# Performance work log

Hardware: AMD Instinct MI355X
Metric: run time of the kernel (lower is better)

The kernel has to match this reference:

```python
import jax, jax.numpy as jnp
import numpy as np

SOFTMAX_T = 0.01
TOPK_CLIP = 3
SCORE_THR = 0.01
IOU_THR = 0.5
CLIP_RATIO = 0.65
OBJ_RATIO = 0.35
PRE_TOP = 1000   # pre-NMS candidates kept from the N*C (proposal, class) grid
MAX_OUT = 300    # max detections per image (padded)


def setup_inputs() -> dict:
    key = jax.random.key(0)
    k1, k2, k3, k4, k5 = jax.random.split(key, 5)
    B, N, D, C = 8, 1000, 512, 1203
    pe = jax.random.normal(k1, (B, N, D), jnp.float32)
    obj = jax.random.uniform(k2, (B, N), jnp.float32)
    xy = jax.random.uniform(k3, (B, N, 2), jnp.float32) * 900.0
    wh = jax.random.uniform(k4, (B, N, 2), jnp.float32) * 100.0 + 1.0
    boxes = jnp.concatenate([xy, xy + wh], axis=-1)  # valid x1y1x2y2
    ce = jax.random.normal(k5, (C, D), jnp.float32)
    image_ids = jnp.arange(B, dtype=jnp.int32)
    return {"proposal_embeddings": pe, "proposal_objectness": obj,
            "proposal_bboxes": boxes, "class_embeddings": ce,
            "image_ids": image_ids}


def _pairwise_iou(b):
    # b: [K, 4] in x1y1x2y2
    x1, y1, x2, y2 = b[:, 0], b[:, 1], b[:, 2], b[:, 3]
    area = jnp.maximum(x2 - x1, 0.0) * jnp.maximum(y2 - y1, 0.0)
    iw = jnp.maximum(jnp.minimum(x2[:, None], x2[None, :]) - jnp.maximum(x1[:, None], x1[None, :]), 0.0)
    ih = jnp.maximum(jnp.minimum(y2[:, None], y2[None, :]) - jnp.maximum(y1[:, None], y1[None, :]), 0.0)
    inter = iw * ih
    union = area[:, None] + area[None, :] - inter
    return inter / jnp.maximum(union, 1e-6)


def _nms_single(boxes, scores):
    # boxes: [N, 4], scores: [N, C] -> fixed-shape multiclass NMS
    N, C = scores.shape
    flat = scores.reshape(-1)                      # [N*C]
    s = jnp.where(flat > SCORE_THR, flat, -1.0)
    top_s, top_i = jax.lax.top_k(s, PRE_TOP)       # sorted desc
    lab = top_i % C
    pid = top_i // C
    b = boxes[pid]                                 # [K, 4]
    valid = top_s > SCORE_THR
    iou = _pairwise_iou(b)                         # [K, K]
    sup_mat = (iou > IOU_THR) & (lab[:, None] == lab[None, :])
    idx = jnp.arange(PRE_TOP)

    def body(i, keep):
        sup = sup_mat[i] & keep[i] & (idx > i)     # a kept box suppresses lower-scored same-class overlaps
        return keep & ~sup

    keep = jax.lax.fori_loop(0, PRE_TOP, body, valid)
    kept = jnp.where(keep, top_s, -1.0)
    fs, fi = jax.lax.top_k(kept, MAX_OUT)
    fvalid = fs > SCORE_THR
    fb = jnp.where(fvalid[:, None], b[fi], 0.0)
    bbox5 = jnp.concatenate([fb, jnp.where(fvalid, fs, 0.0)[:, None]], axis=-1)
    flab = jnp.where(fvalid, lab[fi], -1)
    return bbox5, flab, fvalid


def reference(proposal_embeddings, proposal_objectness, proposal_bboxes, class_embeddings, image_ids):
    pe = proposal_embeddings / jnp.linalg.norm(proposal_embeddings, axis=2, keepdims=True)
    logit = jax.nn.softmax(jnp.einsum('bnd,cd->bnc', pe, class_embeddings) / SOFTMAX_T, axis=2)
    v = jax.lax.top_k(logit, TOPK_CLIP)[0]         # [B, N, TOPK]
    clip_k = logit * (logit >= v[..., -1:])
    final = clip_k * CLIP_RATIO + (clip_k > 0) * proposal_objectness[..., None] * OBJ_RATIO
    bbox5, labels, valid = jax.vmap(_nms_single)(proposal_bboxes, final)
    img = jnp.where(valid, image_ids[:, None], -1)
    B = bbox5.shape[0]
    return bbox5.reshape(B * MAX_OUT, 5), labels.reshape(-1), img.reshape(-1)
```

## Files before the change

kernel.cpp:

```cpp
#include <hip/hip_runtime.h>
#include <stdint.h>

typedef unsigned long long u64;
typedef unsigned int u32;

#define BIMG 8
#define NPROP 1000
#define DDIM 512
#define CCLS 1203
#define MAXOUT 300
#define CSLOT 4096
#define TRIW 8665
#define CTI 1204

__device__ __forceinline__ u32 flipf(float f) {
  u32 u = __float_as_uint(f);
  return (u & 0x80000000u) ? ~u : (u | 0x80000000u);
}
__device__ __forceinline__ float unflipf(u32 x) {
  u32 u = (x & 0x80000000u) ? (x ^ 0x80000000u) : ~x;
  return __uint_as_float(u);
}
__device__ __forceinline__ void push3(float v, float& a0, float& a1, float& a2) {
  if (v > a0) { a2 = a1; a1 = a0; a0 = v; }
  else if (v > a1) { a2 = a1; a1 = v; }
  else if (v > a2) { a2 = v; }
}

__global__ __launch_bounds__(128) void transpose_cei(
    const float* __restrict__ ce, float4* __restrict__ ceTi)
{
  const int c = blockIdx.x;
  const int t = threadIdx.x;
  float4 v = *((const float4*)(ce + (size_t)c * DDIM) + t);
  ceTi[(size_t)t * CTI + c] = v;
}

__global__ __launch_bounds__(512) void score_kernel_i(
    const float* __restrict__ pe, const float* __restrict__ obj,
    const float4* __restrict__ ceTi, u64* __restrict__ cand)
{
  __shared__ float pe_s[8][DDIM];
  __shared__ float red2[8];
  __shared__ float trip2[8][3];
  __shared__ u64 rowc[8][16];
  __shared__ u32 rcnt[8];

  const int tid = threadIdx.x;
  const int lane = tid & 63, wv = tid >> 6;
  const int blk = blockIdx.x;
  const int b = blk / 125;
  const int n0 = (blk % 125) * 8;

  {
    const float4* src = (const float4*)(pe + (size_t)(b * NPROP + n0) * DDIM);
    float4* dst = (float4*)&pe_s[0][0];
    for (int i = tid; i < 1024; i += 512) dst[i] = src[i];
  }
  if (tid < 8) rcnt[tid] = 0u;
  __syncthreads();

  float nrm[8];
  #pragma unroll 1
  for (int r = 0; r < 8; r++) {
    float s = 0.f;
    if (tid < 256) {
      float x0 = pe_s[r][tid], x1 = pe_s[r][tid + 256];
      s = x0 * x0 + x1 * x1;
    }
    #pragma unroll
    for (int off = 32; off; off >>= 1) s += __shfl_xor(s, off);
    if (lane == 0 && wv < 4) red2[wv] = s;
    __syncthreads();
    nrm[r] = sqrtf(((red2[0] + red2[1]) + red2[2]) + red2[3]);
    __syncthreads();
  }
  if (tid < 256) {
    #pragma unroll
    for (int r = 0; r < 8; r++) {
      pe_s[r][tid]       = __fdiv_rn(pe_s[r][tid], nrm[r]);
      pe_s[r][tid + 256] = __fdiv_rn(pe_s[r][tid + 256], nrm[r]);
    }
  }
  __syncthreads();

  const bool has3 = (tid < 179);
  const int c2c = has3 ? (1024 + tid) : 1202;

  float acc[3][8];
  #pragma unroll
  for (int k = 0; k < 3; k++)
    #pragma unroll
    for (int r = 0; r < 8; r++) acc[k][r] = 0.f;

  const float4* ps4 = (const float4*)&pe_s[0][0];
  const float4* pA = ceTi + tid;
  const float4* pB = ceTi + 512 + tid;
  const float4* pC = ceTi + c2c;
  for (int d4 = 0; d4 < 128; d4++) {
    float4 bA = pA[(size_t)d4 * CTI];
    float4 bB = pB[(size_t)d4 * CTI];
    float4 bC = pC[(size_t)d4 * CTI];
    #pragma unroll
    for (int r = 0; r < 8; r++) {
      float4 a = ps4[r * 128 + d4];
      acc[0][r] = fmaf(a.x, bA.x, acc[0][r]); acc[0][r] = fmaf(a.y, bA.y, acc[0][r]);
      acc[0][r] = fmaf(a.z, bA.z, acc[0][r]); acc[0][r] = fmaf(a.w, bA.w, acc[0][r]);
      acc[1][r] = fmaf(a.x, bB.x, acc[1][r]); acc[1][r] = fmaf(a.y, bB.y, acc[1][r]);
      acc[1][r] = fmaf(a.z, bB.z, acc[1][r]); acc[1][r] = fmaf(a.w, bB.w, acc[1][r]);
      acc[2][r] = fmaf(a.x, bC.x, acc[2][r]); acc[2][r] = fmaf(a.y, bC.y, acc[2][r]);
      acc[2][r] = fmaf(a.z, bC.z, acc[2][r]); acc[2][r] = fmaf(a.w, bC.w, acc[2][r]);
    }
  }

  #pragma unroll
  for (int k = 0; k < 3; k++)
    #pragma unroll
    for (int r = 0; r < 8; r++) acc[k][r] = __fdiv_rn(acc[k][r], 0.01f);

  #pragma unroll 1
  for (int r = 0; r < 8; r++) {
    const float l0 = acc[0][r], l1 = acc[1][r];
    const float l2 = has3 ? acc[2][r] : -INFINITY;

    float t0 = -INFINITY, t1 = -INFINITY, t2 = -INFINITY;
    push3(l0, t0, t1, t2); push3(l1, t0, t1, t2); push3(l2, t0, t1, t2);
    #pragma unroll
    for (int off = 32; off; off >>= 1) {
      float u0 = __shfl_xor(t0, off);
      float u1 = __shfl_xor(t1, off);
      float u2 = __shfl_xor(t2, off);
      push3(u0, t0, t1, t2); push3(u1, t0, t1, t2); push3(u2, t0, t1, t2);
    }
    if (lane == 0) { trip2[wv][0] = t0; trip2[wv][1] = t1; trip2[wv][2] = t2; }
    __syncthreads();
    float a0 = -INFINITY, a1 = -INFINITY, a2 = -INFINITY;
    #pragma unroll
    for (int w = 0; w < 8; w++) {
      push3(trip2[w][0], a0, a1, a2);
      push3(trip2[w][1], a0, a1, a2);
      push3(trip2[w][2], a0, a1, a2);
    }
    const float m = a0, s3 = a2;

    float ls = expf(l0 - m);
    ls += expf(l1 - m);
    ls += expf(l2 - m);
    #pragma unroll
    for (int off = 32; off; off >>= 1) ls += __shfl_xor(ls, off);
    if (lane == 0) red2[wv] = ls;
    __syncthreads();
    float sm = red2[0];
    #pragma unroll
    for (int w = 1; w < 8; w++) sm += red2[w];

    const float v3 = __fdiv_rn(expf(s3 - m), sm);
    const float objv = obj[b * NPROP + n0 + r];

    #pragma unroll
    for (int k = 0; k < 3; k++) {
      if (k == 2 && !has3) continue;
      const float lk = (k == 0) ? l0 : (k == 1) ? l1 : l2;
      const float p = __fdiv_rn(expf(lk - m), sm);
      if (p >= v3 && p > 0.f) {
        const float sc = __fadd_rn(__fmul_rn(p, 0.65f), __fmul_rn(objv, 0.35f));
        if (sc > 0.01f) {
          const int c = (k == 0) ? tid : (k == 1) ? (512 + tid) : (1024 + tid);
          u32 flat = (u32)(n0 + r) * (u32)CCLS + (u32)c;
          u64 key = (((u64)flipf(sc)) << 32) | (u32)(~flat);
          u32 slot = atomicAdd(&rcnt[r], 1u);
          if (slot < 16u) rowc[r][slot] = key;
        }
      }
    }
    __syncthreads();
  }

  if (tid < 8) {
    int n = (int)rcnt[tid]; if (n > 16) n = 16;
    for (int a3 = 1; a3 < n; a3++) {
      u64 kx = rowc[tid][a3]; int bp = a3 - 1;
      while (bp >= 0 && rowc[tid][bp] < kx) { rowc[tid][bp + 1] = rowc[tid][bp]; bp--; }
      rowc[tid][bp + 1] = kx;
    }
    int mth = n < 4 ? n : 4;
    u64* dst = cand + (size_t)b * CSLOT + (size_t)(n0 + tid) * 4;
    for (int s2 = 0; s2 < mth; s2++) dst[s2] = rowc[tid][s2];
  }
}

__global__ __launch_bounds__(256, 2) void score_kernel(
    const float* __restrict__ pe, const float* __restrict__ obj,
    const float* __restrict__ ce, u64* __restrict__ cand)
{
  __shared__ float pe_s[8][DDIM];
  __shared__ float red[4][8];
  __shared__ float trip[4][8][3];
  __shared__ u64 rowc[8][16];
  __shared__ u32 rcnt[8];

  const int tid = threadIdx.x;
  const int lane = tid & 63, wv = tid >> 6;
  const int blk = blockIdx.x;
  const int b = blk / 125;
  const int n0 = (blk % 125) * 8;

  {
    const float4* src = (const float4*)(pe + (size_t)(b * NPROP + n0) * DDIM);
    float4* dst = (float4*)&pe_s[0][0];
    for (int i = tid; i < 1024; i += 256) dst[i] = src[i];
  }
  if (tid < 8) rcnt[tid] = 0u;
  __syncthreads();

  float nrm[8];
  #pragma unroll
  for (int r = 0; r < 8; r++) {
    float x0 = pe_s[r][tid], x1 = pe_s[r][tid + 256];
    float s = x0 * x0 + x1 * x1;
    #pragma unroll
    for (int off = 32; off; off >>= 1) s += __shfl_xor(s, off);
    if (lane == 0) red[wv][r] = s;
  }
  __syncthreads();
  #pragma unroll
  for (int r = 0; r < 8; r++)
    nrm[r] = sqrtf(((red[0][r] + red[1][r]) + red[2][r]) + red[3][r]);
  __syncthreads();
  #pragma unroll
  for (int r = 0; r < 8; r++) {
    pe_s[r][tid]       = __fdiv_rn(pe_s[r][tid], nrm[r]);
    pe_s[r][tid + 256] = __fdiv_rn(pe_s[r][tid + 256], nrm[r]);
  }
  __syncthreads();

  const int c4 = 1024 + tid;
  const bool v4 = (c4 < CCLS);
  const float4* ceb = (const float4*)ce;
  const float4* pc0 = ceb + (size_t)(tid)       * 128;
  const float4* pc1 = ceb + (size_t)(tid + 256) * 128;
  const float4* pc2 = ceb + (size_t)(tid + 512) * 128;
  const float4* pc3 = ceb + (size_t)(tid + 768) * 128;
  const float4* pc4 = ceb + (size_t)(v4 ? c4 : (CCLS - 1)) * 128;

  float acc[5][8];
  #pragma unroll
  for (int k = 0; k < 5; k++)
    #pragma unroll
    for (int r = 0; r < 8; r++) acc[k][r] = 0.f;

  const float4* ps4 = (const float4*)&pe_s[0][0];
  for (int d4 = 0; d4 < 128; d4++) {
    float4 bv0 = pc0[d4], bv1 = pc1[d4], bv2 = pc2[d4], bv3 = pc3[d4], bv4 = pc4[d4];
    #pragma unroll
    for (int r = 0; r < 8; r++) {
      float4 a = ps4[r * 128 + d4];
      acc[0][r] = fmaf(a.x, bv0.x, acc[0][r]); acc[0][r] = fmaf(a.y, bv0.y, acc[0][r]);
      acc[0][r] = fmaf(a.z, bv0.z, acc[0][r]); acc[0][r] = fmaf(a.w, bv0.w, acc[0][r]);
      acc[1][r] = fmaf(a.x, bv1.x, acc[1][r]); acc[1][r] = fmaf(a.y, bv1.y, acc[1][r]);
      acc[1][r] = fmaf(a.z, bv1.z, acc[1][r]); acc[1][r] = fmaf(a.w, bv1.w, acc[1][r]);
      acc[2][r] = fmaf(a.x, bv2.x, acc[2][r]); acc[2][r] = fmaf(a.y, bv2.y, acc[2][r]);
      acc[2][r] = fmaf(a.z, bv2.z, acc[2][r]); acc[2][r] = fmaf(a.w, bv2.w, acc[2][r]);
      acc[3][r] = fmaf(a.x, bv3.x, acc[3][r]); acc[3][r] = fmaf(a.y, bv3.y, acc[3][r]);
      acc[3][r] = fmaf(a.z, bv3.z, acc[3][r]); acc[3][r] = fmaf(a.w, bv3.w, acc[3][r]);
      acc[4][r] = fmaf(a.x, bv4.x, acc[4][r]); acc[4][r] = fmaf(a.y, bv4.y, acc[4][r]);
      acc[4][r] = fmaf(a.z, bv4.z, acc[4][r]); acc[4][r] = fmaf(a.w, bv4.w, acc[4][r]);
    }
  }

  #pragma unroll
  for (int k = 0; k < 5; k++)
    #pragma unroll
    for (int r = 0; r < 8; r++) acc[k][r] = __fdiv_rn(acc[k][r], 0.01f);
  if (!v4) {
    #pragma unroll
    for (int r = 0; r < 8; r++) acc[4][r] = -INFINITY;
  }

  float t0[8], t1[8], t2[8];
  #pragma unroll
  for (int r = 0; r < 8; r++) {
    t0[r] = t1[r] = t2[r] = -INFINITY;
    push3(acc[0][r], t0[r], t1[r], t2[r]);
    push3(acc[1][r], t0[r], t1[r], t2[r]);
    push3(acc[2][r], t0[r], t1[r], t2[r]);
    push3(acc[3][r], t0[r], t1[r], t2[r]);
    push3(acc[4][r], t0[r], t1[r], t2[r]);
  }
  #pragma unroll
  for (int off = 32; off; off >>= 1) {
    #pragma unroll
    for (int r = 0; r < 8; r++) {
      float u0 = __shfl_xor(t0[r], off);
      float u1 = __shfl_xor(t1[r], off);
      float u2 = __shfl_xor(t2[r], off);
      push3(u0, t0[r], t1[r], t2[r]);
      push3(u1, t0[r], t1[r], t2[r]);
      push3(u2, t0[r], t1[r], t2[r]);
    }
  }
  if (lane == 0) {
    #pragma unroll
    for (int r = 0; r < 8; r++) {
      trip[wv][r][0] = t0[r]; trip[wv][r][1] = t1[r]; trip[wv][r][2] = t2[r];
    }
  }
  __syncthreads();
  float m[8], s3[8];
  #pragma unroll
  for (int r = 0; r < 8; r++) {
    float a0 = -INFINITY, a1 = -INFINITY, a2 = -INFINITY;
    #pragma unroll
    for (int w = 0; w < 4; w++) {
      push3(trip[w][r][0], a0, a1, a2);
      push3(trip[w][r][1], a0, a1, a2);
      push3(trip[w][r][2], a0, a1, a2);
    }
    m[r] = a0; s3[r] = a2;
  }

  float sm[8];
  #pragma unroll
  for (int r = 0; r < 8; r++) {
    float ls = expf(acc[0][r] - m[r]);
    ls += expf(acc[1][r] - m[r]);
    ls += expf(acc[2][r] - m[r]);
    ls += expf(acc[3][r] - m[r]);
    ls += expf(acc[4][r] - m[r]);
    #pragma unroll
    for (int off = 32; off; off >>= 1) ls += __shfl_xor(ls, off);
    if (lane == 0) red[wv][r] = ls;
  }
  __syncthreads();
  #pragma unroll
  for (int r = 0; r < 8; r++)
    sm[r] = ((red[0][r] + red[1][r]) + red[2][r]) + red[3][r];

  float v3[8], objv[8];
  #pragma unroll
  for (int r = 0; r < 8; r++) {
    v3[r] = __fdiv_rn(expf(s3[r] - m[r]), sm[r]);
    objv[r] = obj[b * NPROP + n0 + r];
  }

  #pragma unroll
  for (int k = 0; k < 5; k++) {
    if (k == 4 && !v4) continue;
    const int c = tid + (k << 8);
    #pragma unroll
    for (int r = 0; r < 8; r++) {
      float e = expf(acc[k][r] - m[r]);
      float p = __fdiv_rn(e, sm[r]);
      if (p >= v3[r] && p > 0.f) {
        float sc = __fadd_rn(__fmul_rn(p, 0.65f), __fmul_rn(objv[r], 0.35f));
        if (sc > 0.01f) {
          u32 flat = (u32)(n0 + r) * (u32)CCLS + (u32)c;
          u64 key = (((u64)flipf(sc)) << 32) | (u32)(~flat);
          u32 slot = atomicAdd(&rcnt[r], 1u);
          if (slot < 16u) rowc[r][slot] = key;
        }
      }
    }
  }
  __syncthreads();
  if (tid < 8) {
    int n = (int)rcnt[tid]; if (n > 16) n = 16;
    for (int a2 = 1; a2 < n; a2++) {
      u64 kx = rowc[tid][a2]; int bp = a2 - 1;
      while (bp >= 0 && rowc[tid][bp] < kx) { rowc[tid][bp + 1] = rowc[tid][bp]; bp--; }
      rowc[tid][bp + 1] = kx;
    }
    int mth = n < 4 ? n : 4;
    u64* dst = cand + (size_t)b * CSLOT + (size_t)(n0 + tid) * 4;
    for (int s2 = 0; s2 < mth; s2++) dst[s2] = rowc[tid][s2];
  }
}

__global__ __launch_bounds__(1024) void sort_kernel(u64* __restrict__ cand)
{
  __shared__ u64 s[CSLOT];
  const int tid = threadIdx.x;
  u64* cb = cand + (size_t)blockIdx.x * CSLOT;
  for (int i = tid; i < CSLOT; i += 1024) s[i] = cb[i];
  __syncthreads();
  for (int k = 2; k <= CSLOT; k <<= 1) {
    for (int j = k >> 1; j > 0; j >>= 1) {
      for (int i = tid; i < CSLOT; i += 1024) {
        int ixj = i ^ j;
        if (ixj > i) {
          u64 a = s[i], c = s[ixj];
          if (((i & k) == 0) ? (a < c) : (a > c)) { s[i] = c; s[ixj] = a; }
        }
      }
      __syncthreads();
    }
  }
  for (int i = tid; i < CSLOT; i += 1024) cb[i] = s[i];
}

__global__ __launch_bounds__(1024) void nms_fused(
    const u64* __restrict__ cand, const float* __restrict__ boxes,
    const int* __restrict__ image_ids, float* __restrict__ out)
{
  __shared__ u64 supw[TRIW];
  __shared__ float4 bx[NPROP];
  __shared__ float ar[NPROP];
  __shared__ float scs[NPROP];
  __shared__ int lbs[NPROP];

  const int tid = threadIdx.x;
  const int b = blockIdx.x;

  for (int i = tid; i < NPROP; i += 1024) {
    u64 key = cand[(size_t)b * CSLOT + i];
    float sc = -1.0f; int pid = 0, lab = -1;
    if (key != 0ull) {
      sc = unflipf((u32)(key >> 32));
      u32 flat = ~(u32)key;
      pid = (int)(flat / (u32)CCLS);
      lab = (int)(flat % (u32)CCLS);
    }
    float4 v = ((const float4*)boxes)[b * NPROP + pid];
    bx[i] = v;
    ar[i] = __fmul_rn(fmaxf(__fsub_rn(v.z, v.x), 0.f),
                      fmaxf(__fsub_rn(v.w, v.y), 0.f));
    scs[i] = sc;
    lbs[i] = lab;
  }
  __syncthreads();

  for (int i = tid; i < NPROP; i += 1024) {
    float4 bi = bx[i]; float ai = ar[i]; int li = lbs[i];
    int g = i >> 6, t = i - (g << 6);
    int rb = 16 * i - (32 * g * (g - 1) + g * (t + 1));
    int w0 = (i + 1) >> 6;
    for (int w = w0; w < 16; w++) {
      u64 bits = 0;
      int jb = w << 6;
      int ts = (w == g) ? (t + 1) : 0;
      int te = NPROP - jb; if (te > 64) te = 64;
      for (int tt = ts; tt < te; tt++) {
        int j = jb + tt;
        if (lbs[j] != li) continue;
        float4 bj = bx[j];
        float iw = fmaxf(__fsub_rn(fminf(bi.z, bj.z), fmaxf(bi.x, bj.x)), 0.f);
        float ih = fmaxf(__fsub_rn(fminf(bi.w, bj.w), fmaxf(bi.y, bj.y)), 0.f);
        float inter = __fmul_rn(iw, ih);
        if (inter <= 0.f) continue;
        float uni = __fsub_rn(__fadd_rn(ai, ar[j]), inter);
        if (__fdiv_rn(inter, fmaxf(uni, 1e-6f)) > 0.5f) bits |= (1ull << tt);
      }
      supw[rb + w - w0] = bits;
    }
  }
  __syncthreads();

  for (int j = tid; j < MAXOUT * 5; j += 1024)
    out[(size_t)b * MAXOUT * 5 + j] = 0.f;
  for (int j = tid; j < MAXOUT; j += 1024) {
    out[BIMG * MAXOUT * 5 + b * MAXOUT + j] = -1.f;
    out[BIMG * MAXOUT * 6 + b * MAXOUT + j] = -1.f;
  }
  __syncthreads();

  if (tid >= 64) return;
  const int lane = tid, myw = lane & 15;

  u64 keep = 0;
  if (lane < 16) {
    #pragma unroll 4
    for (int t = 0; t < 64; t++) {
      int i = (lane << 6) + t;
      if (i < NPROP && scs[i] > 0.01f) keep |= (1ull << t);
    }
  }

  auto LDROW = [&](int i) -> u64 {
    if (i >= NPROP || lane >= 16) return 0ull;
    int g = i >> 6, t = i & 63;
    int w0 = (i + 1) >> 6;
    if (myw < w0) return 0ull;
    int rb = 16 * i - (32 * g * (g - 1) + g * (t + 1));
    return supw[rb + myw - w0];
  };

  u64 p0 = LDROW(0), p1 = LDROW(1), p2 = LDROW(2), p3 = LDROW(3);
  for (int i = 0; i < NPROP; i += 4) {
    #pragma unroll
    for (int q = 0; q < 4; q++) {
      u64 row = (q == 0) ? p0 : (q == 1) ? p1 : (q == 2) ? p2 : p3;
      int ii = i + q;
      int wi = ii >> 6, ti = ii & 63;
      u32 klo = __shfl((u32)keep, wi);
      u32 khi = __shfl((u32)(keep >> 32), wi);
      u64 kword = (((u64)khi) << 32) | klo;
      if ((kword >> ti) & 1ull) keep &= ~row;
      u64 nxt = LDROW(ii + 4);
      if (q == 0) p0 = nxt; else if (q == 1) p1 = nxt; else if (q == 2) p2 = nxt; else p3 = nxt;
    }
  }

  int cntk = (lane < 16) ? __popcll(keep) : 0;
  int inc = cntk;
  #pragma unroll
  for (int off = 1; off < 64; off <<= 1) {
    int v = __shfl_up(inc, off);
    if (lane >= off) inc += v;
  }
  int pre = inc - cntk;
  float imgv = (float)image_ids[b];

  if (lane < 16) {
    int rank = pre;
    u64 kk = keep;
    while (kk) {
      int t = __builtin_ctzll(kk);
      kk &= kk - 1;
      int i = (lane << 6) + t;
      if (rank < MAXOUT) {
        float4 bv = bx[i];
        size_t ro = (size_t)(b * MAXOUT + rank) * 5;
        out[ro + 0] = bv.x;
        out[ro + 1] = bv.y;
        out[ro + 2] = bv.z;
        out[ro + 3] = bv.w;
        out[ro + 4] = scs[i];
        out[BIMG * MAXOUT * 5 + b * MAXOUT + rank] = (float)lbs[i];
        out[BIMG * MAXOUT * 6 + b * MAXOUT + rank] = imgv;
      }
      rank++;
    }
  }
}

extern "C" void kernel_launch(void* const* d_in, const int* in_sizes, int n_in,
                              void* d_out, int out_size, void* d_ws, size_t ws_size,
                              hipStream_t stream) {
  (void)in_sizes; (void)n_in; (void)out_size;
  const float* pe = (const float*)d_in[0];
  const float* obj = (const float*)d_in[1];
  const float* boxes = (const float*)d_in[2];
  const float* ce = (const float*)d_in[3];
  const int* image_ids = (const int*)d_in[4];
  float* out = (float*)d_out;

  const size_t candB = (size_t)BIMG * CSLOT * sizeof(u64);
  const size_t ceTiB = (size_t)128 * CTI * sizeof(float4);
  u64* cand = (u64*)d_ws;
  float4* ceTi = (float4*)((char*)d_ws + candB);

  hipMemsetAsync(cand, 0, candB, stream);
  if (ws_size >= candB + ceTiB) {
    transpose_cei<<<dim3(CCLS), dim3(128), 0, stream>>>(ce, ceTi);
    score_kernel_i<<<dim3(1000), dim3(512), 0, stream>>>(pe, obj, ceTi, cand);
  } else {
    score_kernel<<<dim3(1000), dim3(256), 0, stream>>>(pe, obj, ce, cand);
  }
  sort_kernel<<<dim3(BIMG), dim3(1024), 0, stream>>>(cand);
  nms_fused<<<dim3(BIMG), dim3(1024), 0, stream>>>(cand, boxes, image_ids, out);
}
```

Measured before the change: 672.1 us.

## Pre-normalize proposal embeddings and read them from global memory in scoring kernel

Adds a separate normalize_pe kernel that writes L2-normalized embeddings to workspace, and a new score kernel that reads those rows directly from global memory instead of staging them in shared memory. Normalization and LDS staging are removed from the scoring loop, and the A operand is read with uniform broadcast loads through cache. In exchange there is an extra kernel launch and an extra write and read of a 16 MB buffer. The padding of ceTi grows by one row so the new path reads stay in bounds.

```diff
diff --git a/kernel.cpp b/kernel.cpp
--- a/kernel.cpp
+++ b/kernel.cpp
@@ -34,6 +34,151 @@
   const int t = threadIdx.x;
   float4 v = *((const float4*)(ce + (size_t)c * DDIM) + t);
   ceTi[(size_t)t * CTI + c] = v;
+}
+
+__global__ __launch_bounds__(256) void normalize_pe(
+    const float* __restrict__ pe, float* __restrict__ peN)
+{
+  __shared__ float red[4];
+  const int tid = threadIdx.x;
+  const int lane = tid & 63, wv = tid >> 6;
+  const size_t base = (size_t)blockIdx.x * DDIM;
+  float x0 = pe[base + tid];
+  float x1 = pe[base + tid + 256];
+  float s = x0 * x0 + x1 * x1;
+  #pragma unroll
+  for (int off = 32; off; off >>= 1) s += __shfl_xor(s, off);
+  if (lane == 0) red[wv] = s;
+  __syncthreads();
+  float nrm = sqrtf(((red[0] + red[1]) + red[2]) + red[3]);
+  peN[base + tid]       = __fdiv_rn(x0, nrm);
+  peN[base + tid + 256] = __fdiv_rn(x1, nrm);
+}
+
+__global__ __launch_bounds__(512) void score_kernel_g(
+    const float* __restrict__ peN, const float* __restrict__ obj,
+    const float4* __restrict__ ceTi, u64* __restrict__ cand)
+{
+  __shared__ float red2[8];
+  __shared__ float trip2[8][3];
+  __shared__ u64 rowc[8][16];
+  __shared__ u32 rcnt[8];
+
+  const int tid = threadIdx.x;
+  const int lane = tid & 63, wv = tid >> 6;
+  const int blk = blockIdx.x;
+  const int b = blk / 125;
+  const int n0 = (blk % 125) * 8;
+
+  if (tid < 8) rcnt[tid] = 0u;
+  __syncthreads();
+
+  const bool has3 = (tid < 179);
+  const int c2c = has3 ? (1024 + tid) : 1202;
+
+  float acc[3][8];
+  #pragma unroll
+  for (int k = 0; k < 3; k++)
+    #pragma unroll
+    for (int r = 0; r < 8; r++) acc[k][r] = 0.f;
+
+  const float4* aBase = (const float4*)(peN + (size_t)(b * NPROP + n0) * DDIM);
+  const float4* pA = ceTi + tid;
+  const float4* pB = ceTi + 512 + tid;
+  const float4* pC = ceTi + c2c;
+
+  #pragma unroll 1
+  for (int d4 = 0; d4 < 128; d4++) {
+    const size_t o = (size_t)d4 * CTI;
+    float4 bA = pA[o];
+    float4 bB = pB[o];
+    float4 bC = pC[o];
+    #pragma unroll
+    for (int r = 0; r < 8; r++) {
+      float4 a = aBase[r * 128 + d4];
+      acc[0][r] = fmaf(a.x, bA.x, acc[0][r]); acc[0][r] = fmaf(a.y, bA.y, acc[0][r]);
+      acc[0][r] = fmaf(a.z, bA.z, acc[0][r]); acc[0][r] = fmaf(a.w, bA.w, acc[0][r]);
+      acc[1][r] = fmaf(a.x, bB.x, acc[1][r]); acc[1][r] = fmaf(a.y, bB.y, acc[1][r]);
+      acc[1][r] = fmaf(a.z, bB.z, acc[1][r]); acc[1][r] = fmaf(a.w, bB.w, acc[1][r]);
+      acc[2][r] = fmaf(a.x, bC.x, acc[2][r]); acc[2][r] = fmaf(a.y, bC.y, acc[2][r]);
+      acc[2][r] = fmaf(a.z, bC.z, acc[2][r]); acc[2][r] = fmaf(a.w, bC.w, acc[2][r]);
+    }
+  }
+
+  #pragma unroll
+  for (int k = 0; k < 3; k++)
+    #pragma unroll
+    for (int r = 0; r < 8; r++) acc[k][r] = __fdiv_rn(acc[k][r], 0.01f);
+
+  #pragma unroll 1
+  for (int r = 0; r < 8; r++) {
+    const float l0 = acc[0][r], l1 = acc[1][r];
+    const float l2 = has3 ? acc[2][r] : -INFINITY;
+
+    float t0 = -INFINITY, t1 = -INFINITY, t2 = -INFINITY;
+    push3(l0, t0, t1, t2); push3(l1, t0, t1, t2); push3(l2, t0, t1, t2);
+    #pragma unroll
+    for (int off = 32; off; off >>= 1) {
+      float u0 = __shfl_xor(t0, off);
+      float u1 = __shfl_xor(t1, off);
+      float u2 = __shfl_xor(t2, off);
+      push3(u0, t0, t1, t2); push3(u1, t0, t1, t2); push3(u2, t0, t1, t2);
+    }
+    if (lane == 0) { trip2[wv][0] = t0; trip2[wv][1] = t1; trip2[wv][2] = t2; }
+    __syncthreads();
+    float a0 = -INFINITY, a1 = -INFINITY, a2 = -INFINITY;
+    #pragma unroll
+    for (int w = 0; w < 8; w++) {
+      push3(trip2[w][0], a0, a1, a2);
+      push3(trip2[w][1], a0, a1, a2);
+      push3(trip2[w][2], a0, a1, a2);
+    }
+    const float m = a0, s3 = a2;
+
+    float ls = expf(l0 - m);
+    ls += expf(l1 - m);
+    ls += expf(l2 - m);
+    #pragma unroll
+    for (int off = 32; off; off >>= 1) ls += __shfl_xor(ls, off);
+    if (lane == 0) red2[wv] = ls;
+    __syncthreads();
+    float sm = red2[0];
+    #pragma unroll
+    for (int w = 1; w < 8; w++) sm += red2[w];
+
+    const float v3 = __fdiv_rn(expf(s3 - m), sm);
+    const float objv = obj[b * NPROP + n0 + r];
+
+    #pragma unroll
+    for (int k = 0; k < 3; k++) {
+      if (k == 2 && !has3) continue;
+      const float lk = (k == 0) ? l0 : (k == 1) ? l1 : l2;
+      const float p = __fdiv_rn(expf(lk - m), sm);
+      if (p >= v3 && p > 0.f) {
+        const float sc = __fadd_rn(__fmul_rn(p, 0.65f), __fmul_rn(objv, 0.35f));
+        if (sc > 0.01f) {
+          const int c = (k == 0) ? tid : (k == 1) ? (512 + tid) : (1024 + tid);
+          u32 flat = (u32)(n0 + r) * (u32)CCLS + (u32)c;
+          u64 key = (((u64)flipf(sc)) << 32) | (u32)(~flat);
+          u32 slot = atomicAdd(&rcnt[r], 1u);
+          if (slot < 16u) rowc[r][slot] = key;
+        }
+      }
+    }
+    __syncthreads();
+  }
+
+  if (tid < 8) {
+    int n = (int)rcnt[tid]; if (n > 16) n = 16;
+    for (int a3 = 1; a3 < n; a3++) {
+      u64 kx = rowc[tid][a3]; int bp = a3 - 1;
+      while (bp >= 0 && rowc[tid][bp] < kx) { rowc[tid][bp + 1] = rowc[tid][bp]; bp--; }
+      rowc[tid][bp + 1] = kx;
+    }
+    int mth = n < 4 ? n : 4;
+    u64* dst = cand + (size_t)b * CSLOT + (size_t)(n0 + tid) * 4;
+    for (int s2 = 0; s2 < mth; s2++) dst[s2] = rowc[tid][s2];
+  }
 }
 
 __global__ __launch_bounds__(512) void score_kernel_i(
@@ -545,12 +690,18 @@
   float* out = (float*)d_out;
 
   const size_t candB = (size_t)BIMG * CSLOT * sizeof(u64);
-  const size_t ceTiB = (size_t)128 * CTI * sizeof(float4);
+  const size_t ceTiB = (size_t)129 * CTI * sizeof(float4);
+  const size_t peNB  = (size_t)BIMG * NPROP * DDIM * sizeof(float);
   u64* cand = (u64*)d_ws;
   float4* ceTi = (float4*)((char*)d_ws + candB);
+  float* peN = (float*)((char*)d_ws + candB + ceTiB);
 
   hipMemsetAsync(cand, 0, candB, stream);
-  if (ws_size >= candB + ceTiB) {
+  if (ws_size >= candB + ceTiB + peNB) {
+    transpose_cei<<<dim3(CCLS), dim3(128), 0, stream>>>(ce, ceTi);
+    normalize_pe<<<dim3(BIMG * NPROP), dim3(256), 0, stream>>>(pe, peN);
+    score_kernel_g<<<dim3(1000), dim3(512), 0, stream>>>(peN, obj, ceTi, cand);
+  } else if (ws_size >= candB + ceTiB) {
     transpose_cei<<<dim3(CCLS), dim3(128), 0, stream>>>(ce, ceTi);
     score_kernel_i<<<dim3(1000), dim3(512), 0, stream>>>(pe, obj, ceTi, cand);
   } else {
```

After: 614.1 us. 8.6% less time.
